# Kernel optimization log

Hardware: AMD Instinct MI355X
Metric: run time of the kernel (lower is better)

Reference implementation:

```python
import jax, jax.numpy as jnp
import numpy as np

EMBED_DIM = 1024
NUM_HEADS = 16
HEAD_DIM = EMBED_DIM // NUM_HEADS


def setup_inputs() -> dict:
    key = jax.random.key(0)
    k1, k2, k3, k4 = jax.random.split(key, 4)
    B, S, D = 2, 2048, EMBED_DIM
    x = jax.random.normal(k1, (B, S, D), dtype=jnp.float32)
    xpos = jax.random.randint(k2, (B, S), 0, 2048, dtype=jnp.int32)
    # torch nn.Linear weights: [out_features, in_features]; qkv_bias=False -> no qkv bias
    qkv_w = jax.random.normal(k3, (3 * D, D), dtype=jnp.float32) * (D ** -0.5)
    proj_w = jax.random.normal(k4, (D, D), dtype=jnp.float32) * (D ** -0.5)
    proj_b = jnp.zeros((D,), dtype=jnp.float32)
    return {"x": x, "xpos": xpos, "qkv_w": qkv_w, "proj_w": proj_w, "proj_b": proj_b}


def reference(x, xpos, qkv_w, proj_w, proj_b):
    # rope is None, dropout rates are 0, so xpos is unused and dropout is identity.
    B, S, D = x.shape
    H, hd = NUM_HEADS, D // NUM_HEADS
    scale = hd ** -0.5

    qkv = x @ qkv_w.T                                   # [B, S, 3D]
    qkv = qkv.reshape(B, S, 3, H, hd)
    qkv = jnp.transpose(qkv, (0, 3, 2, 1, 4))           # [B, H, 3, S, hd]
    q, k, v = qkv[:, :, 0], qkv[:, :, 1], qkv[:, :, 2]  # each [B, H, S, hd]

    scores = jnp.einsum("bhqd,bhkd->bhqk", q, k) * scale  # [B, H, S, S]
    probs = jax.nn.softmax(scores, axis=-1)
    out = jnp.einsum("bhqk,bhkd->bhqd", probs, v)         # [B, H, S, hd]

    out = jnp.transpose(out, (0, 2, 1, 3)).reshape(B, S, D)
    out = out @ proj_w.T + proj_b
    return out
```

## Files before the change

### kernel.cpp

```cpp
#include <hip/hip_runtime.h>


typedef __bf16 bf16_8 __attribute__((ext_vector_type(8)));
typedef __bf16 bf16_4 __attribute__((ext_vector_type(4)));
typedef float floatx4 __attribute__((ext_vector_type(4)));

#define MFMA16 __builtin_amdgcn_mfma_f32_16x16x32_bf16
#define CSCALE 0.1803368801111204f

__device__ __forceinline__ void gld16(const __bf16* g, __bf16* l) {
    __builtin_amdgcn_global_load_lds(
        (const __attribute__((address_space(1))) void*)g,
        (__attribute__((address_space(3))) void*)l, 16, 0, 0);
}

__global__ __launch_bounds__(256) void cvt_f32_bf16(
    const float* __restrict__ src, __bf16* __restrict__ dst, int n4)
{
    int i = blockIdx.x * 256 + threadIdx.x;
    if (i < n4) {
        float4 v = ((const float4*)src)[i];
        bf16_4 o;
        o[0] = (__bf16)v.x; o[1] = (__bf16)v.y; o[2] = (__bf16)v.z; o[3] = (__bf16)v.w;
        ((bf16_4*)dst)[i] = o;
    }
}

__device__ __forceinline__ void gemm_bt_mainloop(
    const __bf16* __restrict__ A, const __bf16* __restrict__ B,
    int K, __bf16* As, __bf16* Bs, floatx4 (&acc)[4][4])
{
    const int tid  = threadIdx.x;
    const int lane = tid & 63;
    const int wv   = tid >> 6;
    const int quad = lane >> 4;
    const int l15  = lane & 15;
    const int wm   = (wv >> 1) * 64;
    const int wn   = (wv & 1) * 64;

    for (int k0 = 0; k0 < K; k0 += 64) {
        __syncthreads();
#pragma unroll
        for (int it = 0; it < 4; ++it) {
            int cc = it * 256 + tid;
            int row = cc >> 3, kc = cc & 7;
            gld16(A + row * K + k0 + ((kc ^ (row & 7)) * 8), &As[cc * 8]);
        }
#pragma unroll
        for (int it = 0; it < 4; ++it) {
            int cc = it * 256 + tid;
            int row = cc >> 3, kc = cc & 7;
            gld16(B + row * K + k0 + ((kc ^ (row & 7)) * 8), &Bs[cc * 8]);
        }
        __syncthreads();

#pragma unroll
        for (int ks = 0; ks < 2; ++ks) {
            bf16_8 af[4], bf[4];
#pragma unroll
            for (int mt = 0; mt < 4; ++mt) {
                int r = wm + mt * 16 + l15;
                af[mt] = *(const bf16_8*)&As[r * 64 + (((ks * 4 + quad) ^ (r & 7)) * 8)];
            }
#pragma unroll
            for (int nt = 0; nt < 4; ++nt) {
                int r = wn + nt * 16 + l15;
                bf[nt] = *(const bf16_8*)&Bs[r * 64 + (((ks * 4 + quad) ^ (r & 7)) * 8)];
            }
#pragma unroll
            for (int mt = 0; mt < 4; ++mt)
#pragma unroll
                for (int nt = 0; nt < 4; ++nt)
                    acc[mt][nt] = MFMA16(af[mt], bf[nt], acc[mt][nt], 0, 0, 0);
        }
    }
}

__global__ __launch_bounds__(256) void qkv_gemm(
    const __bf16* __restrict__ X, const __bf16* __restrict__ W,
    __bf16* __restrict__ q_ws, __bf16* __restrict__ k_ws, __bf16* __restrict__ vt_ws)
{
    __shared__ __align__(16) __bf16 As[128 * 64];
    __shared__ __align__(16) __bf16 Bs[128 * 64];
    floatx4 acc[4][4] = {};
    const int m0 = blockIdx.y * 128, n0 = blockIdx.x * 128;
    const int c = n0 >> 10;

    const int tid = threadIdx.x, lane = tid & 63, wv = tid >> 6;
    const int quad = lane >> 4, l15 = lane & 15;
    const int wm = (wv >> 1) * 64, wn = (wv & 1) * 64;

    if (c == 2) {
        gemm_bt_mainloop(X + (size_t)m0 * 1024, W + (size_t)n0 * 1024, 1024, As, Bs, acc);
#pragma unroll
        for (int mt = 0; mt < 4; ++mt) {
            const int mbase = m0 + wm + mt * 16 + quad * 4;
            const int b = mbase >> 11, s = mbase & 2047;
#pragma unroll
            for (int nt = 0; nt < 4; ++nt) {
                const int n = n0 + wn + nt * 16 + l15;
                const int h = (n >> 6) & 15, d = n & 63;
                bf16_4 pk;
#pragma unroll
                for (int r = 0; r < 4; ++r) pk[r] = (__bf16)acc[mt][nt][r];
                *(bf16_4*)&vt_ws[((b * 16 + h) * 64 + d) * 2048 + s] = pk;
            }
        }
    } else {
        gemm_bt_mainloop(W + (size_t)n0 * 1024, X + (size_t)m0 * 1024, 1024, As, Bs, acc);
        __bf16* dst = (c == 0) ? q_ws : k_ws;
        const float scale = (c == 1) ? CSCALE : 1.0f;
#pragma unroll
        for (int mt = 0; mt < 4; ++mt) {
            const int nn = n0 + wm + mt * 16 + quad * 4;
            const int h = (nn >> 6) & 15, d0 = nn & 63;
#pragma unroll
            for (int nt = 0; nt < 4; ++nt) {
                const int token = m0 + wn + nt * 16 + l15;
                const int b = token >> 11, s = token & 2047;
                bf16_4 pk;
#pragma unroll
                for (int r = 0; r < 4; ++r) pk[r] = (__bf16)(acc[mt][nt][r] * scale);
                *(bf16_4*)&dst[((b * 16 + h) * 2048 + s) * 64 + d0] = pk;
            }
        }
    }
}

__global__ __launch_bounds__(256) void attn_kernel(
    const __bf16* __restrict__ q_ws, const __bf16* __restrict__ k_ws,
    const __bf16* __restrict__ vt_ws, __bf16* __restrict__ attn_ws)
{
    __shared__ __align__(16) __bf16 Ks [64 * 64];
    __shared__ __align__(16) __bf16 Vts[64 * 64];
    __shared__ __align__(16) __bf16 Ps [4][2][16][72];

    const int tid = threadIdx.x, lane = tid & 63, w = tid >> 6;
    const int quad = lane >> 4, l15 = lane & 15;
    const int bh = blockIdx.x, qt = blockIdx.y;
    const int q0 = qt * 128;

    const __bf16* qp  = q_ws  + (size_t)bh * (2048 * 64);
    const __bf16* kp  = k_ws  + (size_t)bh * (2048 * 64);
    const __bf16* vtp = vt_ws + (size_t)bh * (64 * 2048);

    bf16_8 qf[2][2];
#pragma unroll
    for (int qg = 0; qg < 2; ++qg) {
        const int qrow = q0 + w * 32 + qg * 16 + l15;
        qf[qg][0] = *(const bf16_8*)&qp[qrow * 64 + quad * 8];
        qf[qg][1] = *(const bf16_8*)&qp[qrow * 64 + 32 + quad * 8];
    }

    floatx4 oacc[2][4] = {};
    float l_part[2] = {0.f, 0.f};

    for (int kt = 0; kt < 32; ++kt) {
        const int ktok = kt * 64;
        __syncthreads();
#pragma unroll
        for (int it = 0; it < 2; ++it) {
            int cc = it * 256 + tid;
            int row = cc >> 3, kc = cc & 7;
            gld16(kp + (ktok + row) * 64 + ((kc ^ (row & 7)) * 8), &Ks[cc * 8]);
        }
#pragma unroll
        for (int it = 0; it < 2; ++it) {
            int cc = it * 256 + tid;
            int row = cc >> 3, kc = cc & 7;
            gld16(vtp + row * 2048 + ktok + ((kc ^ (row & 7)) * 8), &Vts[cc * 8]);
        }
        __syncthreads();

        floatx4 sacc[2][4] = {};
#pragma unroll
        for (int ks = 0; ks < 2; ++ks)
#pragma unroll
            for (int kg = 0; kg < 4; ++kg) {
                int krow = kg * 16 + l15;
                bf16_8 kf = *(const bf16_8*)&Ks[krow * 64 + (((ks * 4 + quad) ^ (krow & 7)) * 8)];
                sacc[0][kg] = MFMA16(kf, qf[0][ks], sacc[0][kg], 0, 0, 0);
                sacc[1][kg] = MFMA16(kf, qf[1][ks], sacc[1][kg], 0, 0, 0);
            }

#pragma unroll
        for (int qg = 0; qg < 2; ++qg)
#pragma unroll
            for (int kg = 0; kg < 4; ++kg) {
                bf16_4 pk;
                float e0 = exp2f(sacc[qg][kg][0]);
                float e1 = exp2f(sacc[qg][kg][1]);
                float e2 = exp2f(sacc[qg][kg][2]);
                float e3 = exp2f(sacc[qg][kg][3]);
                l_part[qg] += (e0 + e1) + (e2 + e3);
                pk[0] = (__bf16)e0; pk[1] = (__bf16)e1;
                pk[2] = (__bf16)e2; pk[3] = (__bf16)e3;
                *(bf16_4*)&Ps[w][qg][l15][kg * 16 + quad * 4] = pk;
            }
        __asm__ __volatile__("s_waitcnt lgkmcnt(0)" ::: "memory");

#pragma unroll
        for (int ks = 0; ks < 2; ++ks) {
            bf16_8 pf0 = *(const bf16_8*)&Ps[w][0][l15][ks * 32 + quad * 8];
            bf16_8 pf1 = *(const bf16_8*)&Ps[w][1][l15][ks * 32 + quad * 8];
#pragma unroll
            for (int dg = 0; dg < 4; ++dg) {
                int drow = dg * 16 + l15;
                bf16_8 vf = *(const bf16_8*)&Vts[drow * 64 + (((ks * 4 + quad) ^ (drow & 7)) * 8)];
                oacc[0][dg] = MFMA16(vf, pf0, oacc[0][dg], 0, 0, 0);
                oacc[1][dg] = MFMA16(vf, pf1, oacc[1][dg], 0, 0, 0);
            }
        }
    }

    const int b = bh >> 4, h = bh & 15;
#pragma unroll
    for (int qg = 0; qg < 2; ++qg) {
        float l = l_part[qg];
        l += __shfl_xor(l, 16);
        l += __shfl_xor(l, 32);
        const float inv_l = 1.0f / l;
        const int token = b * 2048 + q0 + w * 32 + qg * 16 + l15;
#pragma unroll
        for (int dg = 0; dg < 4; ++dg) {
            bf16_4 ok;
#pragma unroll
            for (int r = 0; r < 4; ++r) ok[r] = (__bf16)(oacc[qg][dg][r] * inv_l);
            *(bf16_4*)&attn_ws[(size_t)token * 1024 + h * 64 + dg * 16 + quad * 4] = ok;
        }
    }
}

__global__ __launch_bounds__(256) void proj_gemm(
    const __bf16* __restrict__ Ain, const __bf16* __restrict__ W,
    const float* __restrict__ bias, float* __restrict__ out)
{
    __shared__ __align__(16) __bf16 As[128 * 64];
    __shared__ __align__(16) __bf16 Bs[128 * 64];
    floatx4 acc[4][4] = {};
    const int m0 = blockIdx.y * 128, n0 = blockIdx.x * 128;

    gemm_bt_mainloop(Ain + (size_t)m0 * 1024, W + (size_t)n0 * 1024, 1024, As, Bs, acc);

    const int tid = threadIdx.x, lane = tid & 63, wv = tid >> 6;
    const int quad = lane >> 4, l15 = lane & 15;
    const int wm = (wv >> 1) * 64, wn = (wv & 1) * 64;

    float bv[4];
#pragma unroll
    for (int nt = 0; nt < 4; ++nt) bv[nt] = bias[n0 + wn + nt * 16 + l15];

#pragma unroll
    for (int mt = 0; mt < 4; ++mt) {
        const int m = m0 + wm + mt * 16 + quad * 4;
#pragma unroll
        for (int nt = 0; nt < 4; ++nt) {
            const int n = n0 + wn + nt * 16 + l15;
#pragma unroll
            for (int r = 0; r < 4; ++r)
                out[(size_t)(m + r) * 1024 + n] = acc[mt][nt][r] + bv[nt];
        }
    }
}

extern "C" void kernel_launch(void* const* d_in, const int* in_sizes, int n_in,
                              void* d_out, int out_size, void* d_ws, size_t ws_size,
                              hipStream_t stream)
{
    const float* x      = (const float*)d_in[0];
    const float* qkv_w  = (const float*)d_in[2];
    const float* proj_w = (const float*)d_in[3];
    const float* proj_b = (const float*)d_in[4];
    float* out = (float*)d_out;

    const size_t SZ   = 4096 * 1024;
    const size_t WQKV = 3072 * 1024;
    const size_t WPRJ = 1024 * 1024;

    __bf16* xb      = (__bf16*)d_ws;
    __bf16* qkvwb   = xb + SZ;
    __bf16* projwb  = qkvwb + WQKV;
    __bf16* q_ws    = projwb + WPRJ;
    __bf16* k_ws    = q_ws + SZ;
    __bf16* vt_ws   = k_ws + SZ;
    __bf16* attn_ws = vt_ws + SZ;

    cvt_f32_bf16<<<dim3(SZ / 4 / 256),   256, 0, stream>>>(x,      xb,     SZ / 4);
    cvt_f32_bf16<<<dim3(WQKV / 4 / 256), 256, 0, stream>>>(qkv_w,  qkvwb,  WQKV / 4);
    cvt_f32_bf16<<<dim3(WPRJ / 4 / 256), 256, 0, stream>>>(proj_w, projwb, WPRJ / 4);

    qkv_gemm  <<<dim3(24, 32), 256, 0, stream>>>(xb, qkvwb, q_ws, k_ws, vt_ws);
    attn_kernel<<<dim3(32, 16), 256, 0, stream>>>(q_ws, k_ws, vt_ws, attn_ws);
    proj_gemm <<<dim3(8, 32), 256, 0, stream>>>(attn_ws, projwb, proj_b, out);
}
```

Measured before the change: 216.9 us.

## Double-buffer K/V tiles in attention and merge conversion kernels into one launch

The attention kernel now holds two LDS buffers for the K and V^T tiles. It issues the async global-to-LDS load for tile kt+1 before computing on tile kt, so load latency overlaps the MFMA and exp work and one barrier per iteration is removed. The three fp32-to-bf16 conversion launches become a single kernel that picks its source by index range, which saves launch overhead and tail effects. LDS use in attention grows by 16 KB per block, which could lower occupancy.

Result: faster. 210.6 us (-2.9%).

```diff
diff --git a/kernel.cpp b/kernel.cpp
--- a/kernel.cpp
+++ b/kernel.cpp
@@ -14,16 +14,20 @@
         (__attribute__((address_space(3))) void*)l, 16, 0, 0);
 }
 
-__global__ __launch_bounds__(256) void cvt_f32_bf16(
-    const float* __restrict__ src, __bf16* __restrict__ dst, int n4)
-{
-    int i = blockIdx.x * 256 + threadIdx.x;
-    if (i < n4) {
-        float4 v = ((const float4*)src)[i];
-        bf16_4 o;
-        o[0] = (__bf16)v.x; o[1] = (__bf16)v.y; o[2] = (__bf16)v.z; o[3] = (__bf16)v.w;
-        ((bf16_4*)dst)[i] = o;
-    }
+__global__ __launch_bounds__(256) void cvt_all(
+    const float* __restrict__ x, const float* __restrict__ w1,
+    const float* __restrict__ w2,
+    __bf16* __restrict__ xb, __bf16* __restrict__ w1b, __bf16* __restrict__ w2b)
+{
+    const int i = blockIdx.x * 256 + threadIdx.x;
+    const float* src; __bf16* dst; int off;
+    if (i < (1 << 20))                  { src = x;  dst = xb;  off = i; }
+    else if (i < (1 << 20) + 786432)    { src = w1; dst = w1b; off = i - (1 << 20); }
+    else                                { src = w2; dst = w2b; off = i - (1 << 20) - 786432; }
+    float4 v = ((const float4*)src)[off];
+    bf16_4 o;
+    o[0] = (__bf16)v.x; o[1] = (__bf16)v.y; o[2] = (__bf16)v.z; o[3] = (__bf16)v.w;
+    ((bf16_4*)dst)[off] = o;
 }
 
 __device__ __forceinline__ void gemm_bt_mainloop(
@@ -131,8 +135,8 @@
     const __bf16* __restrict__ q_ws, const __bf16* __restrict__ k_ws,
     const __bf16* __restrict__ vt_ws, __bf16* __restrict__ attn_ws)
 {
-    __shared__ __align__(16) __bf16 Ks [64 * 64];
-    __shared__ __align__(16) __bf16 Vts[64 * 64];
+    __shared__ __align__(16) __bf16 Ks [2][64 * 64];
+    __shared__ __align__(16) __bf16 Vts[2][64 * 64];
     __shared__ __align__(16) __bf16 Ps [4][2][16][72];
 
     const int tid = threadIdx.x, lane = tid & 63, w = tid >> 6;
@@ -144,6 +148,23 @@
     const __bf16* kp  = k_ws  + (size_t)bh * (2048 * 64);
     const __bf16* vtp = vt_ws + (size_t)bh * (64 * 2048);
 
+    const int srow = tid >> 3, skc = tid & 7;
+    const int sslot = (skc ^ (srow & 7)) * 8;
+    auto stage = [&](int buf, int ktok) {
+#pragma unroll
+        for (int it = 0; it < 2; ++it) {
+            int row = srow + it * 32;
+            gld16(kp + (ktok + row) * 64 + ((skc ^ (row & 7)) * 8),
+                  &Ks[buf][(row * 8 + skc) * 8]);
+        }
+#pragma unroll
+        for (int it = 0; it < 2; ++it) {
+            int row = srow + it * 32;
+            gld16(vtp + row * 2048 + ktok + ((skc ^ (row & 7)) * 8),
+                  &Vts[buf][(row * 8 + skc) * 8]);
+        }
+    };
+
     bf16_8 qf[2][2];
 #pragma unroll
     for (int qg = 0; qg < 2; ++qg) {
@@ -155,22 +176,15 @@
     floatx4 oacc[2][4] = {};
     float l_part[2] = {0.f, 0.f};
 
+    stage(0, 0);
+
     for (int kt = 0; kt < 32; ++kt) {
-        const int ktok = kt * 64;
+        const int cur = kt & 1;
         __syncthreads();
-#pragma unroll
-        for (int it = 0; it < 2; ++it) {
-            int cc = it * 256 + tid;
-            int row = cc >> 3, kc = cc & 7;
-            gld16(kp + (ktok + row) * 64 + ((kc ^ (row & 7)) * 8), &Ks[cc * 8]);
-        }
-#pragma unroll
-        for (int it = 0; it < 2; ++it) {
-            int cc = it * 256 + tid;
-            int row = cc >> 3, kc = cc & 7;
-            gld16(vtp + row * 2048 + ktok + ((kc ^ (row & 7)) * 8), &Vts[cc * 8]);
-        }
-        __syncthreads();
+        if (kt + 1 < 32) stage(cur ^ 1, (kt + 1) * 64);
+
+        const __bf16* Kb = Ks[cur];
+        const __bf16* Vb = Vts[cur];
 
         floatx4 sacc[2][4] = {};
 #pragma unroll
@@ -178,7 +192,7 @@
 #pragma unroll
             for (int kg = 0; kg < 4; ++kg) {
                 int krow = kg * 16 + l15;
-                bf16_8 kf = *(const bf16_8*)&Ks[krow * 64 + (((ks * 4 + quad) ^ (krow & 7)) * 8)];
+                bf16_8 kf = *(const bf16_8*)&Kb[krow * 64 + (((ks * 4 + quad) ^ (krow & 7)) * 8)];
                 sacc[0][kg] = MFMA16(kf, qf[0][ks], sacc[0][kg], 0, 0, 0);
                 sacc[1][kg] = MFMA16(kf, qf[1][ks], sacc[1][kg], 0, 0, 0);
             }
@@ -206,7 +220,7 @@
 #pragma unroll
             for (int dg = 0; dg < 4; ++dg) {
                 int drow = dg * 16 + l15;
-                bf16_8 vf = *(const bf16_8*)&Vts[drow * 64 + (((ks * 4 + quad) ^ (drow & 7)) * 8)];
+                bf16_8 vf = *(const bf16_8*)&Vb[drow * 64 + (((ks * 4 + quad) ^ (drow & 7)) * 8)];
                 oacc[0][dg] = MFMA16(vf, pf0, oacc[0][dg], 0, 0, 0);
                 oacc[1][dg] = MFMA16(vf, pf1, oacc[1][dg], 0, 0, 0);
             }
@@ -285,10 +299,7 @@
     __bf16* vt_ws   = k_ws + SZ;
     __bf16* attn_ws = vt_ws + SZ;
 
-    cvt_f32_bf16<<<dim3(SZ / 4 / 256),   256, 0, stream>>>(x,      xb,     SZ / 4);
-    cvt_f32_bf16<<<dim3(WQKV / 4 / 256), 256, 0, stream>>>(qkv_w,  qkvwb,  WQKV / 4);
-    cvt_f32_bf16<<<dim3(WPRJ / 4 / 256), 256, 0, stream>>>(proj_w, projwb, WPRJ / 4);
-
+    cvt_all<<<dim3(8192), 256, 0, stream>>>(x, qkv_w, proj_w, xb, qkvwb, projwb);
     qkv_gemm  <<<dim3(24, 32), 256, 0, stream>>>(xb, qkvwb, q_ws, k_ws, vt_ws);
     attn_kernel<<<dim3(32, 16), 256, 0, stream>>>(q_ws, k_ws, vt_ws, attn_ws);
     proj_gemm <<<dim3(8, 32), 256, 0, stream>>>(attn_ws, projwb, proj_b, out);
```
